# Kernel tuning notes

Hardware: AMD Instinct MI355X
Metric: run time of the kernel (lower is better)

The kernel has to match this reference:

```python
import jax, jax.numpy as jnp
import numpy as np

HEADS = 16
DIM_HEAD = 64
SCALE = DIM_HEAD ** (-0.5)


def setup_inputs() -> dict:
    key = jax.random.key(0)
    ks = jax.random.split(key, 6)
    B, N, D = 2, 2048, 1024
    inner = HEADS * DIM_HEAD  # 1024
    s = 0.02
    return {
        "x": jax.random.normal(ks[0], (B, N, D), dtype=jnp.float32),
        "Wq": jax.random.normal(ks[1], (D, inner), dtype=jnp.float32) * s,
        "Wk": jax.random.normal(ks[2], (D, inner), dtype=jnp.float32) * s,
        "Wv": jax.random.normal(ks[3], (D, inner), dtype=jnp.float32) * s,
        "Wo": jax.random.normal(ks[4], (inner, D), dtype=jnp.float32) * s,
        "bo": jnp.zeros((D,), dtype=jnp.float32),
    }


def reference(x, Wq, Wk, Wv, Wo, bo):
    B, N, _ = x.shape
    # projections, split heads: [B, N, inner] -> [B, H, N, d]
    def split(t):
        return t.reshape(B, N, HEADS, DIM_HEAD).transpose(0, 2, 1, 3)
    q = split(x @ Wq)
    k = split(x @ Wk)  # self-attention: context = x
    v = split(x @ Wv)
    # scores [B, H, N, N], softmax over keys
    scores = jnp.einsum('bhid,bhjd->bhij', q, k) * SCALE
    attn = jax.nn.softmax(scores, axis=-1)
    out = jnp.einsum('bhij,bhjd->bhid', attn, v)
    out = out.transpose(0, 2, 1, 3).reshape(B, N, HEADS * DIM_HEAD)
    return out @ Wo + bo
```

## Files before the change

### kernel.cpp

```cpp
#include <hip/hip_runtime.h>
#include <hip/hip_bf16.h>
#include <stdint.h>

typedef unsigned short u16;
typedef __attribute__((ext_vector_type(8))) short bf16x8;
typedef __attribute__((ext_vector_type(4))) float f32x4;
typedef __attribute__((ext_vector_type(4))) unsigned int u32x4;

#define QSCALE 0.18033688011112042f

__device__ __forceinline__ u16 f2bf(float f) {
  return __builtin_bit_cast(u16, __float2bfloat16(f));
}

__device__ __forceinline__ uint32_t pkcvt(float a, float b) {
  return (uint32_t)f2bf(a) | ((uint32_t)f2bf(b) << 16);
}

__device__ __forceinline__ void gll16(const void* g, void* l) {
  __builtin_amdgcn_global_load_lds(
      (__attribute__((address_space(1))) void*)(uintptr_t)g,
      (__attribute__((address_space(3))) void*)l, 16, 0, 0);
}

__global__ __launch_bounds__(256)
void cvt_all_kernel(const float* __restrict__ x,
                    const float* __restrict__ Wq, const float* __restrict__ Wk,
                    const float* __restrict__ Wv, const float* __restrict__ Wo,
                    u16* __restrict__ xb, u16* __restrict__ Wqkvt, u16* __restrict__ Wot) {
  __shared__ float tile[32][33];
  const int bid = blockIdx.x, tid = threadIdx.x;
  if (bid < 4096) {
    const int z = bid >> 10, xy = bid & 1023;
    const float* src = (z == 0) ? Wq : (z == 1) ? Wk : (z == 2) ? Wv : Wo;
    const float scale = (z == 0) ? QSCALE : 1.0f;
    u16* dst = (z == 3) ? Wot : (Wqkvt + (size_t)z * 1024 * 1024);
    const int n0 = (xy & 31) * 32, k0 = (xy >> 5) * 32;
    const int tx = tid & 31, ty = tid >> 5;
#pragma unroll
    for (int i = 0; i < 4; ++i)
      tile[ty * 4 + i][tx] = src[(size_t)(k0 + ty * 4 + i) * 1024 + n0 + tx];
    __syncthreads();
#pragma unroll
    for (int i = 0; i < 4; ++i)
      dst[(size_t)(n0 + ty * 4 + i) * 1024 + k0 + tx] = f2bf(tile[tx][ty * 4 + i] * scale);
  } else {
    size_t i = (size_t)(bid - 4096) * 256 + tid;
    const float4* p = (const float4*)x + i * 2;
    float4 a = p[0], b = p[1];
    ushort4 lo, hi;
    lo.x = f2bf(a.x); lo.y = f2bf(a.y); lo.z = f2bf(a.z); lo.w = f2bf(a.w);
    hi.x = f2bf(b.x); hi.y = f2bf(b.y); hi.z = f2bf(b.z); hi.w = f2bf(b.w);
    ((ushort4*)xb)[i * 2]     = lo;
    ((ushort4*)xb)[i * 2 + 1] = hi;
  }
}

__global__ __launch_bounds__(256)
void gemm_qkv_kernel(const u16* __restrict__ A, const u16* __restrict__ Bt,
                     u16* __restrict__ Qb, u16* __restrict__ Kb, u16* __restrict__ Vtb) {
  __shared__ __align__(16) u16 As[2][128 * 32];
  __shared__ __align__(16) u16 Bs[2][128 * 32];
  const int row0 = blockIdx.x * 128, col0 = blockIdx.y * 128;
  const int tid = threadIdx.x, lane = tid & 63, wid = tid >> 6;
  const int wr = (wid >> 1) * 64, wc = (wid & 1) * 64;
  const int lr = lane & 15, lg = lane >> 4;
  const int fsw = (lg ^ ((lr >> 2) & 3)) * 16;

  f32x4 acc[4][4];
#pragma unroll
  for (int m = 0; m < 4; ++m)
#pragma unroll
    for (int n = 0; n < 4; ++n) acc[m][n] = (f32x4){0.f, 0.f, 0.f, 0.f};

  auto stage = [&](int b, int k0) {
#pragma unroll
    for (int i = 0; i < 2; ++i) {
      const int c = tid + i * 256;
      const int row = c >> 2, pos = c & 3;
      const int sp = (pos ^ ((row >> 2) & 3)) * 16;
      gll16((const char*)A  + ((size_t)(row0 + row) * 1024 + k0) * 2 + sp, (char*)As[b] + c * 16);
      gll16((const char*)Bt + ((size_t)(col0 + row) * 1024 + k0) * 2 + sp, (char*)Bs[b] + c * 16);
    }
  };

  stage(0, 0);
  asm volatile("s_waitcnt vmcnt(0)" ::: "memory");
  __syncthreads();

  int buf = 0;
  for (int t = 0; t < 32; ++t) {
    if (t < 31) stage(buf ^ 1, (t + 1) * 32);
    bf16x8 af[4], bfr[4];
#pragma unroll
    for (int m = 0; m < 4; ++m)
      af[m] = *(const bf16x8*)((const char*)As[buf] + (wr + m * 16 + lr) * 64 + fsw);
#pragma unroll
    for (int n = 0; n < 4; ++n)
      bfr[n] = *(const bf16x8*)((const char*)Bs[buf] + (wc + n * 16 + lr) * 64 + fsw);
    __builtin_amdgcn_s_setprio(1);
#pragma unroll
    for (int m = 0; m < 4; ++m)
#pragma unroll
      for (int n = 0; n < 4; ++n)
        acc[m][n] = __builtin_amdgcn_mfma_f32_16x16x32_bf16(af[m], bfr[n], acc[m][n], 0, 0, 0);
    __builtin_amdgcn_s_setprio(0);
    asm volatile("s_waitcnt vmcnt(0)" ::: "memory");
    __syncthreads();
    buf ^= 1;
  }

#pragma unroll
  for (int m = 0; m < 4; ++m) {
#pragma unroll
    for (int n = 0; n < 4; ++n) {
      const int gcol = col0 + wc + n * 16 + lr;
      const int w = gcol >> 10, rem = gcol & 1023;
      const int h = rem >> 6, dd = rem & 63;
      const int grow0 = row0 + wr + m * 16 + lg * 4;
      if (w == 2) {
        const int b0 = grow0 >> 11, nn0 = grow0 & 2047;
        const int kin = nn0 & 63;
        const int kp = (kin & 32) | ((kin & 12) << 1) | ((kin & 16) >> 2);
        ushort4 sv;
        sv.x = f2bf(acc[m][n][0]); sv.y = f2bf(acc[m][n][1]);
        sv.z = f2bf(acc[m][n][2]); sv.w = f2bf(acc[m][n][3]);
        *(ushort4*)&Vtb[((size_t)(b0 * 16 + h) * 64 + dd) * 2048 + (nn0 & ~63) + kp] = sv;
      } else {
#pragma unroll
        for (int r = 0; r < 4; ++r) {
          const int grow = grow0 + r;
          const int b = grow >> 11, nn = grow & 2047;
          const int bh = b * 16 + h;
          const u16 hv = f2bf(acc[m][n][r]);
          if (w == 0) Qb[((size_t)bh * 2048 + nn) * 64 + dd] = hv;
          else        Kb[((size_t)bh * 2048 + nn) * 64 + dd] = hv;
        }
      }
    }
  }
}

__global__ __launch_bounds__(256, 2)
void attn_kernel(const u16* __restrict__ Qb, const u16* __restrict__ Kb,
                 const u16* __restrict__ Vtb, u16* __restrict__ Ob) {
  __shared__ __align__(16) u16 Ks[2][128 * 64];
  __shared__ __align__(16) u16 Vs[2][128 * 64];
  const int tid = threadIdx.x, lane = tid & 63, wid = tid >> 6;
  const int bid = blockIdx.x;
  const int vv = (bid & 7) * 64 + (bid >> 3);
  const int qt = vv & 15, bh = vv >> 4;
  const int lr = lane & 15, lg = lane >> 4;

  const u16* Qp = Qb + ((size_t)bh * 2048 + qt * 128 + wid * 32) * 64;
  const char* Kg = (const char*)(Kb + (size_t)bh * 2048 * 64);
  const char* Vg = (const char*)(Vtb + (size_t)bh * 64 * 2048);

  bf16x8 aq[2][2];
#pragma unroll
  for (int qc = 0; qc < 2; ++qc)
#pragma unroll
    for (int ks = 0; ks < 2; ++ks)
      aq[qc][ks] = *(const bf16x8*)&Qp[(qc * 16 + lr) * 64 + ks * 32 + lg * 8];

  auto stage = [&](int buf, int kv0) {
#pragma unroll
    for (int i = 0; i < 4; ++i) {
      const int c = tid + i * 256;
      const int row = c >> 3;
      const int sc = ((c & 7) * 16) ^ ((row & 7) << 4);
      gll16(Kg + (size_t)(kv0 + row) * 128 + sc, (char*)Ks[buf] + c * 16);
      gll16(Vg + (size_t)(row & 63) * 4096 + (size_t)(kv0 + (row >> 6) * 64) * 2 + sc,
            (char*)Vs[buf] + c * 16);
    }
  };

  const int swz = (lr & 7) << 4;
  const int xk0 = (lg * 16) ^ swz;
  const int xk1 = (64 + lg * 16) ^ swz;

  f32x4 acco[4][2];
#pragma unroll
  for (int ct = 0; ct < 4; ++ct)
#pragma unroll
    for (int qc = 0; qc < 2; ++qc) acco[ct][qc] = (f32x4){0.f, 0.f, 0.f, 0.f};
  f32x4 lacc[2];
  lacc[0] = (f32x4){0.f, 0.f, 0.f, 0.f};
  lacc[1] = (f32x4){0.f, 0.f, 0.f, 0.f};
  const f32x4 minit = (f32x4){-8.f, -8.f, -8.f, -8.f};
  u32x4 ow;
  ow.x = ow.y = ow.z = ow.w = 0x3F803F80u;
  const bf16x8 ones = __builtin_bit_cast(bf16x8, ow);

  stage(0, 0);
  asm volatile("s_waitcnt vmcnt(0)" ::: "memory");
  __syncthreads();

  int buf = 0;
  for (int t = 0; t < 16; ++t) {
    if (t < 15) stage(buf ^ 1, (t + 1) * 128);
#pragma unroll
    for (int u = 0; u < 2; ++u) {
      const char* kbase = (const char*)Ks[buf] + u * 8192 + lr * 128;
      const char* vbase = (const char*)Vs[buf] + u * 8192 + lr * 128;

      bf16x8 kf[4][2];
#pragma unroll
      for (int kt = 0; kt < 4; ++kt) {
        kf[kt][0] = *(const bf16x8*)(kbase + kt * 2048 + xk0);
        kf[kt][1] = *(const bf16x8*)(kbase + kt * 2048 + xk1);
      }
      f32x4 s[4][2];
      __builtin_amdgcn_s_setprio(1);
#pragma unroll
      for (int kt = 0; kt < 4; ++kt)
#pragma unroll
        for (int qc = 0; qc < 2; ++qc) {
          f32x4 tacc = __builtin_amdgcn_mfma_f32_16x16x32_bf16(kf[kt][0], aq[qc][0], minit, 0, 0, 0);
          s[kt][qc]  = __builtin_amdgcn_mfma_f32_16x16x32_bf16(kf[kt][1], aq[qc][1], tacc, 0, 0, 0);
        }
      __builtin_amdgcn_s_setprio(0);
      bf16x8 pa[2][2];
#pragma unroll
      for (int qc = 0; qc < 2; ++qc) {
#pragma unroll
        for (int kt = 0; kt < 4; ++kt)
#pragma unroll
          for (int r = 0; r < 4; ++r)
            s[kt][qc][r] = __builtin_amdgcn_exp2f(s[kt][qc][r]);
#pragma unroll
        for (int ks = 0; ks < 2; ++ks) {
          u32x4 w;
          w.x = pkcvt(s[2 * ks][qc][0],     s[2 * ks][qc][1]);
          w.y = pkcvt(s[2 * ks][qc][2],     s[2 * ks][qc][3]);
          w.z = pkcvt(s[2 * ks + 1][qc][0], s[2 * ks + 1][qc][1]);
          w.w = pkcvt(s[2 * ks + 1][qc][2], s[2 * ks + 1][qc][3]);
          pa[qc][ks] = __builtin_bit_cast(bf16x8, w);
        }
        lacc[qc] = __builtin_amdgcn_mfma_f32_16x16x32_bf16(ones, pa[qc][0], lacc[qc], 0, 0, 0);
        lacc[qc] = __builtin_amdgcn_mfma_f32_16x16x32_bf16(ones, pa[qc][1], lacc[qc], 0, 0, 0);
      }
      __builtin_amdgcn_s_setprio(1);
#pragma unroll
      for (int ct = 0; ct < 4; ++ct) {
        const char* vb = vbase + ct * 2048;
#pragma unroll
        for (int ks = 0; ks < 2; ++ks) {
          bf16x8 vf = *(const bf16x8*)(vb + ((ks * 64 + lg * 16) ^ swz));
#pragma unroll
          for (int qc = 0; qc < 2; ++qc)
            acco[ct][qc] = __builtin_amdgcn_mfma_f32_16x16x32_bf16(vf, pa[qc][ks], acco[ct][qc], 0, 0, 0);
        }
      }
      __builtin_amdgcn_s_setprio(0);
    }
    asm volatile("s_waitcnt vmcnt(0)" ::: "memory");
    __syncthreads();
    buf ^= 1;
  }

  const int b = bh >> 4, h = bh & 15;
#pragma unroll
  for (int qc = 0; qc < 2; ++qc) {
    const int q = qt * 128 + wid * 32 + qc * 16 + lr;
    const float inv = 1.0f / lacc[qc][0];
#pragma unroll
    for (int ct = 0; ct < 4; ++ct) {
      uint2 st;
      st.x = pkcvt(acco[ct][qc][0] * inv, acco[ct][qc][1] * inv);
      st.y = pkcvt(acco[ct][qc][2] * inv, acco[ct][qc][3] * inv);
      *(uint2*)&Ob[((size_t)b * 2048 + q) * 1024 + h * 64 + ct * 16 + lg * 4] = st;
    }
  }
}

__global__ __launch_bounds__(256)
void gemm_out_kernel(const u16* __restrict__ A, const u16* __restrict__ Bt,
                     const float* __restrict__ bo, float* __restrict__ out) {
  __shared__ __align__(16) u16 As[2][128 * 32];
  __shared__ __align__(16) u16 Bs[2][128 * 32];
  const int row0 = blockIdx.x * 128, col0 = blockIdx.y * 128;
  const int tid = threadIdx.x, lane = tid & 63, wid = tid >> 6;
  const int wr = (wid >> 1) * 64, wc = (wid & 1) * 64;
  const int lr = lane & 15, lg = lane >> 4;
  const int fsw = (lg ^ ((lr >> 2) & 3)) * 16;

  f32x4 acc[4][4];
#pragma unroll
  for (int m = 0; m < 4; ++m)
#pragma unroll
    for (int n = 0; n < 4; ++n) acc[m][n] = (f32x4){0.f, 0.f, 0.f, 0.f};

  auto stage = [&](int b, int k0) {
#pragma unroll
    for (int i = 0; i < 2; ++i) {
      const int c = tid + i * 256;
      const int row = c >> 2, pos = c & 3;
      const int sp = (pos ^ ((row >> 2) & 3)) * 16;
      gll16((const char*)A  + ((size_t)(row0 + row) * 1024 + k0) * 2 + sp, (char*)As[b] + c * 16);
      gll16((const char*)Bt + ((size_t)(col0 + row) * 1024 + k0) * 2 + sp, (char*)Bs[b] + c * 16);
    }
  };

  stage(0, 0);
  asm volatile("s_waitcnt vmcnt(0)" ::: "memory");
  __syncthreads();

  int buf = 0;
  for (int t = 0; t < 32; ++t) {
    if (t < 31) stage(buf ^ 1, (t + 1) * 32);
    bf16x8 af[4], bfr[4];
#pragma unroll
    for (int m = 0; m < 4; ++m)
      af[m] = *(const bf16x8*)((const char*)As[buf] + (wr + m * 16 + lr) * 64 + fsw);
#pragma unroll
    for (int n = 0; n < 4; ++n)
      bfr[n] = *(const bf16x8*)((const char*)Bs[buf] + (wc + n * 16 + lr) * 64 + fsw);
    __builtin_amdgcn_s_setprio(1);
#pragma unroll
    for (int m = 0; m < 4; ++m)
#pragma unroll
      for (int n = 0; n < 4; ++n)
        acc[m][n] = __builtin_amdgcn_mfma_f32_16x16x32_bf16(af[m], bfr[n], acc[m][n], 0, 0, 0);
    __builtin_amdgcn_s_setprio(0);
    asm volatile("s_waitcnt vmcnt(0)" ::: "memory");
    __syncthreads();
    buf ^= 1;
  }

#pragma unroll
  for (int m = 0; m < 4; ++m) {
#pragma unroll
    for (int n = 0; n < 4; ++n) {
      const int gcol = col0 + wc + n * 16 + lr;
      const float bv = bo[gcol];
#pragma unroll
      for (int r = 0; r < 4; ++r) {
        const int grow = row0 + wr + m * 16 + lg * 4 + r;
        out[(size_t)grow * 1024 + gcol] = acc[m][n][r] + bv;
      }
    }
  }
}

extern "C" void kernel_launch(void* const* d_in, const int* in_sizes, int n_in,
                              void* d_out, int out_size, void* d_ws, size_t ws_size,
                              hipStream_t stream) {
  const float* x  = (const float*)d_in[0];
  const float* Wq = (const float*)d_in[1];
  const float* Wk = (const float*)d_in[2];
  const float* Wv = (const float*)d_in[3];
  const float* Wo = (const float*)d_in[4];
  const float* bo = (const float*)d_in[5];
  float* out = (float*)d_out;

  char* ws = (char*)d_ws;
  u16* xb    = (u16*)(ws);
  u16* wqkvt = (u16*)(ws + ((size_t)8  << 20));
  u16* wot   = (u16*)(ws + ((size_t)14 << 20));
  u16* Qb    = (u16*)(ws + ((size_t)16 << 20));
  u16* Kb    = (u16*)(ws + ((size_t)24 << 20));
  u16* Vtb   = (u16*)(ws + ((size_t)32 << 20));
  u16* Ob    = xb;

  hipLaunchKernelGGL(cvt_all_kernel, dim3(6144), dim3(256), 0, stream,
                     x, Wq, Wk, Wv, Wo, xb, wqkvt, wot);
  hipLaunchKernelGGL(gemm_qkv_kernel, dim3(32, 24), dim3(256), 0, stream,
                     xb, wqkvt, Qb, Kb, Vtb);
  hipLaunchKernelGGL(attn_kernel, dim3(512), dim3(256), 0, stream,
                     Qb, Kb, Vtb, Ob);
  hipLaunchKernelGGL(gemm_out_kernel, dim3(32, 8), dim3(256), 0, stream,
                     Ob, wot, bo, out);
}
```

Before: 116.9 us.

## Use 512-thread blocks and BK=64 tiles with XOR swizzle in projection GEMMs

Both projection GEMMs now run 8 waves per 128x128 block, each wave computing a 64x32 sub-tile instead of 64x64. The K step doubles from 32 to 64, with a new 8-way XOR swizzle on the 128-byte LDS rows, which halves the number of barrier/wait iterations. The aim is more waves to hide latency and fewer synchronisations per tile. In exchange each wave loads fragments with lower reuse per MFMA, LDS use doubles to 64KB per block, and the setprio hints are dropped.

```diff
diff --git a/kernel.cpp b/kernel.cpp
--- a/kernel.cpp
+++ b/kernel.cpp
@@ -56,29 +56,29 @@
   }
 }
 
-__global__ __launch_bounds__(256)
+__global__ __launch_bounds__(512, 4)
 void gemm_qkv_kernel(const u16* __restrict__ A, const u16* __restrict__ Bt,
                      u16* __restrict__ Qb, u16* __restrict__ Kb, u16* __restrict__ Vtb) {
-  __shared__ __align__(16) u16 As[2][128 * 32];
-  __shared__ __align__(16) u16 Bs[2][128 * 32];
+  __shared__ __align__(16) u16 As[2][128 * 64];
+  __shared__ __align__(16) u16 Bs[2][128 * 64];
   const int row0 = blockIdx.x * 128, col0 = blockIdx.y * 128;
   const int tid = threadIdx.x, lane = tid & 63, wid = tid >> 6;
-  const int wr = (wid >> 1) * 64, wc = (wid & 1) * 64;
+  const int wr = (wid >> 2) * 64, wc = (wid & 3) * 32;
   const int lr = lane & 15, lg = lane >> 4;
-  const int fsw = (lg ^ ((lr >> 2) & 3)) * 16;
-
-  f32x4 acc[4][4];
+  const int swz = (lr & 7) << 4;
+
+  f32x4 acc[4][2];
 #pragma unroll
   for (int m = 0; m < 4; ++m)
 #pragma unroll
-    for (int n = 0; n < 4; ++n) acc[m][n] = (f32x4){0.f, 0.f, 0.f, 0.f};
+    for (int n = 0; n < 2; ++n) acc[m][n] = (f32x4){0.f, 0.f, 0.f, 0.f};
 
   auto stage = [&](int b, int k0) {
 #pragma unroll
     for (int i = 0; i < 2; ++i) {
-      const int c = tid + i * 256;
-      const int row = c >> 2, pos = c & 3;
-      const int sp = (pos ^ ((row >> 2) & 3)) * 16;
+      const int c = tid + i * 512;
+      const int row = c >> 3;
+      const int sp = ((c & 7) * 16) ^ ((row & 7) << 4);
       gll16((const char*)A  + ((size_t)(row0 + row) * 1024 + k0) * 2 + sp, (char*)As[b] + c * 16);
       gll16((const char*)Bt + ((size_t)(col0 + row) * 1024 + k0) * 2 + sp, (char*)Bs[b] + c * 16);
     }
@@ -89,22 +89,24 @@
   __syncthreads();
 
   int buf = 0;
-  for (int t = 0; t < 32; ++t) {
-    if (t < 31) stage(buf ^ 1, (t + 1) * 32);
-    bf16x8 af[4], bfr[4];
-#pragma unroll
-    for (int m = 0; m < 4; ++m)
-      af[m] = *(const bf16x8*)((const char*)As[buf] + (wr + m * 16 + lr) * 64 + fsw);
-#pragma unroll
-    for (int n = 0; n < 4; ++n)
-      bfr[n] = *(const bf16x8*)((const char*)Bs[buf] + (wc + n * 16 + lr) * 64 + fsw);
-    __builtin_amdgcn_s_setprio(1);
-#pragma unroll
-    for (int m = 0; m < 4; ++m)
-#pragma unroll
-      for (int n = 0; n < 4; ++n)
-        acc[m][n] = __builtin_amdgcn_mfma_f32_16x16x32_bf16(af[m], bfr[n], acc[m][n], 0, 0, 0);
-    __builtin_amdgcn_s_setprio(0);
+  for (int t = 0; t < 16; ++t) {
+    if (t < 15) stage(buf ^ 1, (t + 1) * 64);
+#pragma unroll
+    for (int u = 0; u < 2; ++u) {
+      const int xo = (u * 64 + lg * 16) ^ swz;
+      bf16x8 af[4], bfr[2];
+#pragma unroll
+      for (int m = 0; m < 4; ++m)
+        af[m] = *(const bf16x8*)((const char*)As[buf] + (wr + m * 16 + lr) * 128 + xo);
+#pragma unroll
+      for (int n = 0; n < 2; ++n)
+        bfr[n] = *(const bf16x8*)((const char*)Bs[buf] + (wc + n * 16 + lr) * 128 + xo);
+#pragma unroll
+      for (int m = 0; m < 4; ++m)
+#pragma unroll
+        for (int n = 0; n < 2; ++n)
+          acc[m][n] = __builtin_amdgcn_mfma_f32_16x16x32_bf16(af[m], bfr[n], acc[m][n], 0, 0, 0);
+    }
     asm volatile("s_waitcnt vmcnt(0)" ::: "memory");
     __syncthreads();
     buf ^= 1;
@@ -113,7 +115,7 @@
 #pragma unroll
   for (int m = 0; m < 4; ++m) {
 #pragma unroll
-    for (int n = 0; n < 4; ++n) {
+    for (int n = 0; n < 2; ++n) {
       const int gcol = col0 + wc + n * 16 + lr;
       const int w = gcol >> 10, rem = gcol & 1023;
       const int h = rem >> 6, dd = rem & 63;
@@ -274,29 +276,29 @@
   }
 }
 
-__global__ __launch_bounds__(256)
+__global__ __launch_bounds__(512, 4)
 void gemm_out_kernel(const u16* __restrict__ A, const u16* __restrict__ Bt,
                      const float* __restrict__ bo, float* __restrict__ out) {
-  __shared__ __align__(16) u16 As[2][128 * 32];
-  __shared__ __align__(16) u16 Bs[2][128 * 32];
+  __shared__ __align__(16) u16 As[2][128 * 64];
+  __shared__ __align__(16) u16 Bs[2][128 * 64];
   const int row0 = blockIdx.x * 128, col0 = blockIdx.y * 128;
   const int tid = threadIdx.x, lane = tid & 63, wid = tid >> 6;
-  const int wr = (wid >> 1) * 64, wc = (wid & 1) * 64;
+  const int wr = (wid >> 2) * 64, wc = (wid & 3) * 32;
   const int lr = lane & 15, lg = lane >> 4;
-  const int fsw = (lg ^ ((lr >> 2) & 3)) * 16;
-
-  f32x4 acc[4][4];
+  const int swz = (lr & 7) << 4;
+
+  f32x4 acc[4][2];
 #pragma unroll
   for (int m = 0; m < 4; ++m)
 #pragma unroll
-    for (int n = 0; n < 4; ++n) acc[m][n] = (f32x4){0.f, 0.f, 0.f, 0.f};
+    for (int n = 0; n < 2; ++n) acc[m][n] = (f32x4){0.f, 0.f, 0.f, 0.f};
 
   auto stage = [&](int b, int k0) {
 #pragma unroll
     for (int i = 0; i < 2; ++i) {
-      const int c = tid + i * 256;
-      const int row = c >> 2, pos = c & 3;
-      const int sp = (pos ^ ((row >> 2) & 3)) * 16;
+      const int c = tid + i * 512;
+      const int row = c >> 3;
+      const int sp = ((c & 7) * 16) ^ ((row & 7) << 4);
       gll16((const char*)A  + ((size_t)(row0 + row) * 1024 + k0) * 2 + sp, (char*)As[b] + c * 16);
       gll16((const char*)Bt + ((size_t)(col0 + row) * 1024 + k0) * 2 + sp, (char*)Bs[b] + c * 16);
     }
@@ -307,22 +309,24 @@
   __syncthreads();
 
   int buf = 0;
-  for (int t = 0; t < 32; ++t) {
-    if (t < 31) stage(buf ^ 1, (t + 1) * 32);
-    bf16x8 af[4], bfr[4];
-#pragma unroll
-    for (int m = 0; m < 4; ++m)
-      af[m] = *(const bf16x8*)((const char*)As[buf] + (wr + m * 16 + lr) * 64 + fsw);
-#pragma unroll
-    for (int n = 0; n < 4; ++n)
-      bfr[n] = *(const bf16x8*)((const char*)Bs[buf] + (wc + n * 16 + lr) * 64 + fsw);
-    __builtin_amdgcn_s_setprio(1);
-#pragma unroll
-    for (int m = 0; m < 4; ++m)
-#pragma unroll
-      for (int n = 0; n < 4; ++n)
-        acc[m][n] = __builtin_amdgcn_mfma_f32_16x16x32_bf16(af[m], bfr[n], acc[m][n], 0, 0, 0);
-    __builtin_amdgcn_s_setprio(0);
+  for (int t = 0; t < 16; ++t) {
+    if (t < 15) stage(buf ^ 1, (t + 1) * 64);
+#pragma unroll
+    for (int u = 0; u < 2; ++u) {
+      const int xo = (u * 64 + lg * 16) ^ swz;
+      bf16x8 af[4], bfr[2];
+#pragma unroll
+      for (int m = 0; m < 4; ++m)
+        af[m] = *(const bf16x8*)((const char*)As[buf] + (wr + m * 16 + lr) * 128 + xo);
+#pragma unroll
+      for (int n = 0; n < 2; ++n)
+        bfr[n] = *(const bf16x8*)((const char*)Bs[buf] + (wc + n * 16 + lr) * 128 + xo);
+#pragma unroll
+      for (int m = 0; m < 4; ++m)
+#pragma unroll
+        for (int n = 0; n < 2; ++n)
+          acc[m][n] = __builtin_amdgcn_mfma_f32_16x16x32_bf16(af[m], bfr[n], acc[m][n], 0, 0, 0);
+    }
     asm volatile("s_waitcnt vmcnt(0)" ::: "memory");
     __syncthreads();
     buf ^= 1;
@@ -331,7 +335,7 @@
 #pragma unroll
   for (int m = 0; m < 4; ++m) {
 #pragma unroll
-    for (int n = 0; n < 4; ++n) {
+    for (int n = 0; n < 2; ++n) {
       const int gcol = col0 + wc + n * 16 + lr;
       const float bv = bo[gcol];
 #pragma unroll
@@ -365,10 +369,10 @@
 
   hipLaunchKernelGGL(cvt_all_kernel, dim3(6144), dim3(256), 0, stream,
                      x, Wq, Wk, Wv, Wo, xb, wqkvt, wot);
-  hipLaunchKernelGGL(gemm_qkv_kernel, dim3(32, 24), dim3(256), 0, stream,
+  hipLaunchKernelGGL(gemm_qkv_kernel, dim3(32, 24), dim3(512), 0, stream,
                      xb, wqkvt, Qb, Kb, Vtb);
   hipLaunchKernelGGL(attn_kernel, dim3(512), dim3(256), 0, stream,
                      Qb, Kb, Vtb, Ob);
-  hipLaunchKernelGGL(gemm_out_kernel, dim3(32, 8), dim3(256), 0, stream,
+  hipLaunchKernelGGL(gemm_out_kernel, dim3(32, 8), dim3(512), 0, stream,
                      Ob, wot, bo, out);
 }
```

Result: faster. 107.3 us (-8.2%).
